# Performance work log

Hardware: AMD Instinct MI355X
Metric: run time of the kernel (lower is better)

## Reference

```python
import jax, jax.numpy as jnp
import numpy as np


def setup_inputs() -> dict:
    key = jax.random.key(0)
    k1, k2, k3 = jax.random.split(key, 3)
    batch, d_in, d_out, b = 8192, 4096, 4096, 128
    k_in, k_out = d_in // b, d_out // b  # 32, 32
    x = jax.random.normal(k1, (batch, d_in), dtype=jnp.float32)
    W = jax.random.normal(k2, (k_out, k_in, b), dtype=jnp.float32) * 0.1
    d_bernoulli = jnp.ones((d_in,), dtype=jnp.float32)
    bias = jax.random.normal(k3, (d_out,), dtype=jnp.float32) * 0.1
    return {"x": x, "W": W, "d_bernoulli": d_bernoulli, "bias": bias}


def reference(x, W, d_bernoulli, bias):
    # Block-circulant matmul via FFT convolution theorem, fully batched.
    # W: (k_out, k_in, b); each W[i, j] is the first row of a circulant block.
    batch, d_in = x.shape
    k_out, k_in, b = W.shape
    xd = x * d_bernoulli[None, :]
    # d_in == k_in * b here (divisible), so no padding needed.
    x_blocks = xd.reshape(batch, k_in, b)
    Xf = jnp.fft.fft(x_blocks, axis=-1)               # (batch, k_in, b) complex
    Wf = jnp.conjugate(jnp.fft.fft(W, axis=-1))       # (k_out, k_in, b) complex
    # sum over input blocks j in frequency domain, then one IFFT per output block
    Yf = jnp.einsum("bjn,ijn->bin", Xf, Wf)           # (batch, k_out, b)
    y = jnp.fft.ifft(Yf, axis=-1).real.reshape(batch, k_out * b)
    return y + bias[None, :]
```

## Files before the change

### kernel.cpp

```cpp
#include <hip/hip_runtime.h>
#include <hip/hip_bf16.h>
#include <stdint.h>

typedef __bf16 bf16x8 __attribute__((ext_vector_type(8)));
typedef float  f32x4  __attribute__((ext_vector_type(4)));

#define MDIM 8192
#define NDIM 4096
#define KDIM 4096
#define BM   256
#define BN   256
#define BK   64
#define NT   (KDIM / BK)

__device__ __forceinline__ void lds_load16(const void* gsrc, void* ldst) {
    __builtin_amdgcn_global_load_lds(
        (const __attribute__((address_space(1))) unsigned int*)gsrc,
        (__attribute__((address_space(3)))       unsigned int*)ldst,
        16, 0, 0);
}

__global__ __launch_bounds__(256) void cvt_x(const float* __restrict__ X,
                                             __bf16* __restrict__ Xb) {
    size_t t  = (size_t)blockIdx.x * blockDim.x + threadIdx.x;
    size_t i0 = t * 8;
    float4 a = *(const float4*)(X + i0);
    float4 b = *(const float4*)(X + i0 + 4);
    bf16x8 o;
    o[0] = (__bf16)a.x; o[1] = (__bf16)a.y; o[2] = (__bf16)a.z; o[3] = (__bf16)a.w;
    o[4] = (__bf16)b.x; o[5] = (__bf16)b.y; o[6] = (__bf16)b.z; o[7] = (__bf16)b.w;
    *(bf16x8*)(Xb + i0) = o;
}

__global__ __launch_bounds__(256) void build_bt(const float* __restrict__ W,
                                                const float* __restrict__ d,
                                                __bf16* __restrict__ Bt) {
    int t  = blockIdx.x * blockDim.x + threadIdx.x;
    int c  = t >> 9;
    int k0 = (t & 511) * 8;
    int i  = c  >> 7;
    int j  = k0 >> 7;
    const float* wp = W + ((size_t)i * 32 + j) * 128;
    bf16x8 o;
#pragma unroll
    for (int e = 0; e < 8; ++e) {
        int k = k0 + e;
        float v = wp[(k - c) & 127] * d[k];
        o[e] = (__bf16)v;
    }
    *(bf16x8*)(Bt + (size_t)c * KDIM + k0) = o;
}

__global__ __launch_bounds__(512, 2) void gemm_bc(const __bf16* __restrict__ A,
                                                  const __bf16* __restrict__ Bt,
                                                  const float* __restrict__ bias,
                                                  float* __restrict__ C) {
    __shared__ __align__(16) char lds[2 * 65536];

    const int bid = blockIdx.x;
    const int cpx = gridDim.x >> 3;
    const int swz = (bid & 7) * cpx + (bid >> 3);
    const int ntn = NDIM / BN;
    const int brow = (swz / ntn) * BM;
    const int bcol = (swz % ntn) * BN;

    const int tid  = threadIdx.x;
    const int wid  = tid >> 6;
    const int lane = tid & 63;
    const int wr   = wid >> 2;
    const int wc   = wid & 3;
    const int rlo  = lane & 15;
    const int kg   = lane >> 4;

    const int xorK = (rlo & 7) << 4;
    const int kb0  = ((kg * 16)      ^ xorK);
    const int kb1  = ((64 + kg * 16) ^ xorK);
    const char* bufA0 = lds + wr * 16384 + rlo * 128;
    const char* bufB0 = lds + 32768 + (wc >> 1) * 16384 + ((wc & 1) * 64 + rlo) * 128;

    const int sRow = wid * 8 + (lane >> 3);
    const int sCol = 8 * ((lane & 7) ^ ((lane >> 3) & 7));

    const __bf16* Abase = A  + (size_t)brow * KDIM;
    const __bf16* Bbase = Bt + (size_t)bcol * KDIM;

    auto stageA = [&](int t_, int half, int par_) {
#pragma unroll
        for (int l = 0; l < 2; ++l) {
            const __bf16* gp = Abase + (size_t)(half * 128 + l * 64 + sRow) * KDIM
                               + t_ * 64 + sCol;
            lds_load16(gp, lds + par_ * 65536 + half * 16384 + l * 8192 + wid * 1024);
        }
    };
    auto stageB = [&](int t_, int half, int par_) {
#pragma unroll
        for (int l = 0; l < 2; ++l) {
            const __bf16* gp = Bbase + (size_t)(half * 128 + l * 64 + sRow) * KDIM
                               + t_ * 64 + sCol;
            lds_load16(gp, lds + par_ * 65536 + 32768 + half * 16384 + l * 8192 + wid * 1024);
        }
    };

    f32x4 acc[8][4];
#pragma unroll
    for (int i = 0; i < 8; ++i)
#pragma unroll
        for (int j = 0; j < 4; ++j) acc[i][j] = (f32x4)0.0f;

    stageA(0, 0, 0); stageA(0, 1, 0);
    stageB(0, 0, 0); stageB(0, 1, 0);
    stageB(1, 0, 1); stageB(1, 1, 1);

    bf16x8 bf[4][2];

#define PHASE(q, STAGE_STMT)                                                        \
    {                                                                               \
        bf16x8 a00 = *(const bf16x8*)(bufA + (q) * 4096 +    0 + kb0);              \
        bf16x8 a01 = *(const bf16x8*)(bufA + (q) * 4096 +    0 + kb1);              \
        bf16x8 a10 = *(const bf16x8*)(bufA + (q) * 4096 + 2048 + kb0);              \
        bf16x8 a11 = *(const bf16x8*)(bufA + (q) * 4096 + 2048 + kb1);              \
        STAGE_STMT;                                                                 \
        __builtin_amdgcn_s_barrier();                                               \
        asm volatile("s_waitcnt lgkmcnt(0)" ::: "memory");                          \
        __builtin_amdgcn_s_setprio(1);                                              \
        _Pragma("unroll")                                                           \
        for (int j = 0; j < 4; ++j) {                                               \
            acc[(q)*2+0][j] = __builtin_amdgcn_mfma_f32_16x16x32_bf16(a00, bf[j][0], acc[(q)*2+0][j], 0, 0, 0); \
            acc[(q)*2+0][j] = __builtin_amdgcn_mfma_f32_16x16x32_bf16(a01, bf[j][1], acc[(q)*2+0][j], 0, 0, 0); \
            acc[(q)*2+1][j] = __builtin_amdgcn_mfma_f32_16x16x32_bf16(a10, bf[j][0], acc[(q)*2+1][j], 0, 0, 0); \
            acc[(q)*2+1][j] = __builtin_amdgcn_mfma_f32_16x16x32_bf16(a11, bf[j][1], acc[(q)*2+1][j], 0, 0, 0); \
        }                                                                           \
        __builtin_amdgcn_s_setprio(0);                                              \
    }

    for (int t = 0; t < NT; ++t) {
        const int par = t & 1;
        const char* bufA = bufA0 + par * 65536;
        const char* bufB = bufB0 + par * 65536;

        if (t < NT - 1) {
            asm volatile("s_waitcnt vmcnt(4)" ::: "memory");
        } else {
            asm volatile("s_waitcnt vmcnt(0)" ::: "memory");
        }
        __builtin_amdgcn_s_barrier();

#pragma unroll
        for (int j = 0; j < 4; ++j) {
            bf[j][0] = *(const bf16x8*)(bufB + j * 2048 + kb0);
            bf[j][1] = *(const bf16x8*)(bufB + j * 2048 + kb1);
        }
        PHASE(0, { if (t + 1 < NT) stageA(t + 1, 0, 1 - par); });
        PHASE(1, { if (t + 1 < NT) stageA(t + 1, 1, 1 - par); });
        PHASE(2, { if (t + 2 < NT) stageB(t + 2, 0, par); });
        PHASE(3, { if (t + 2 < NT) stageB(t + 2, 1, par); });
    }
#undef PHASE

#pragma unroll
    for (int j = 0; j < 4; ++j) {
        const int col = bcol + wc * 64 + j * 16 + rlo;
        const float bs = bias[col];
#pragma unroll
        for (int i = 0; i < 8; ++i) {
            const int row = brow + wr * 128 + i * 16 + kg * 4;
#pragma unroll
            for (int r = 0; r < 4; ++r)
                C[(size_t)(row + r) * NDIM + col] = acc[i][j][r] + bs;
        }
    }
}

extern "C" void kernel_launch(void* const* d_in, const int* in_sizes, int n_in,
                              void* d_out, int out_size, void* d_ws, size_t ws_size,
                              hipStream_t stream) {
    const float* x    = (const float*)d_in[0];
    const float* W    = (const float*)d_in[1];
    const float* d    = (const float*)d_in[2];
    const float* bias = (const float*)d_in[3];
    float* y = (float*)d_out;

    __bf16* Xb = (__bf16*)d_ws;
    __bf16* Bt = (__bf16*)((char*)d_ws + (size_t)MDIM * KDIM * 2);

    cvt_x<<<(MDIM * (size_t)KDIM) / 8 / 256, 256, 0, stream>>>(x, Xb);
    build_bt<<<(NDIM * KDIM) / 8 / 256, 256, 0, stream>>>(W, d, Bt);
    gemm_bc<<<(MDIM / BM) * (NDIM / BN), 512, 0, stream>>>(Xb, Bt, bias, y);
}
```

Before: 283.7 us.

## Switch GEMM inner loop to 32x32x16 bf16 MFMA with two-phase schedule

Replaces the 16x16x32 MFMA tiling with 32x32x16 MFMA instructions. Each wave now holds 4x2 accumulators of 16 floats, and the LDS fragment addressing and the epilogue row mapping are reworked to match. The four-phase per-K-step schedule is collapsed into two phases, each with its own barrier and prefetch stage, which cuts barriers and LDS reads per MFMA flop. The larger MFMA shape improves operand reuse from LDS, at the cost of different register pressure and a coarser overlap between LDS loads and compute.

```diff
diff --git a/kernel.cpp b/kernel.cpp
--- a/kernel.cpp
+++ b/kernel.cpp
@@ -2,8 +2,8 @@
 #include <hip/hip_bf16.h>
 #include <stdint.h>
 
-typedef __bf16 bf16x8 __attribute__((ext_vector_type(8)));
-typedef float  f32x4  __attribute__((ext_vector_type(4)));
+typedef __bf16 bf16x8  __attribute__((ext_vector_type(8)));
+typedef float  f32x16  __attribute__((ext_vector_type(16)));
 
 #define MDIM 8192
 #define NDIM 4096
@@ -69,14 +69,13 @@
     const int lane = tid & 63;
     const int wr   = wid >> 2;
     const int wc   = wid & 3;
-    const int rlo  = lane & 15;
-    const int kg   = lane >> 4;
+    const int l31  = lane & 31;
+    const int kh   = lane >> 5;
 
-    const int xorK = (rlo & 7) << 4;
-    const int kb0  = ((kg * 16)      ^ xorK);
-    const int kb1  = ((64 + kg * 16) ^ xorK);
-    const char* bufA0 = lds + wr * 16384 + rlo * 128;
-    const char* bufB0 = lds + 32768 + (wc >> 1) * 16384 + ((wc & 1) * 64 + rlo) * 128;
+    const int kbase = (((l31 & 7) ^ kh) << 4);
+
+    const int aOffBase = (wr * 128 + l31) * 128;
+    const int bOffBase = 32768 + (wc * 64 + l31) * 128;
 
     const int sRow = wid * 8 + (lane >> 3);
     const int sCol = 8 * ((lane & 7) ^ ((lane >> 3) & 7));
@@ -101,72 +100,77 @@
         }
     };
 
-    f32x4 acc[8][4];
+    f32x16 acc[4][2];
 #pragma unroll
-    for (int i = 0; i < 8; ++i)
+    for (int i = 0; i < 4; ++i)
 #pragma unroll
-        for (int j = 0; j < 4; ++j) acc[i][j] = (f32x4)0.0f;
+        for (int j = 0; j < 2; ++j) acc[i][j] = (f32x16)0.0f;
 
     stageA(0, 0, 0); stageA(0, 1, 0);
     stageB(0, 0, 0); stageB(0, 1, 0);
     stageB(1, 0, 1); stageB(1, 1, 1);
 
-    bf16x8 bf[4][2];
+    for (int t = 0; t < NT; ++t) {
+        const int par  = t & 1;
+        const char* buf = lds + par * 65536;
 
-#define PHASE(q, STAGE_STMT)                                                        \
-    {                                                                               \
-        bf16x8 a00 = *(const bf16x8*)(bufA + (q) * 4096 +    0 + kb0);              \
-        bf16x8 a01 = *(const bf16x8*)(bufA + (q) * 4096 +    0 + kb1);              \
-        bf16x8 a10 = *(const bf16x8*)(bufA + (q) * 4096 + 2048 + kb0);              \
-        bf16x8 a11 = *(const bf16x8*)(bufA + (q) * 4096 + 2048 + kb1);              \
-        STAGE_STMT;                                                                 \
-        __builtin_amdgcn_s_barrier();                                               \
-        asm volatile("s_waitcnt lgkmcnt(0)" ::: "memory");                          \
-        __builtin_amdgcn_s_setprio(1);                                              \
-        _Pragma("unroll")                                                           \
-        for (int j = 0; j < 4; ++j) {                                               \
-            acc[(q)*2+0][j] = __builtin_amdgcn_mfma_f32_16x16x32_bf16(a00, bf[j][0], acc[(q)*2+0][j], 0, 0, 0); \
-            acc[(q)*2+0][j] = __builtin_amdgcn_mfma_f32_16x16x32_bf16(a01, bf[j][1], acc[(q)*2+0][j], 0, 0, 0); \
-            acc[(q)*2+1][j] = __builtin_amdgcn_mfma_f32_16x16x32_bf16(a10, bf[j][0], acc[(q)*2+1][j], 0, 0, 0); \
-            acc[(q)*2+1][j] = __builtin_amdgcn_mfma_f32_16x16x32_bf16(a11, bf[j][1], acc[(q)*2+1][j], 0, 0, 0); \
-        }                                                                           \
-        __builtin_amdgcn_s_setprio(0);                                              \
+        if (t < NT - 1) { asm volatile("s_waitcnt vmcnt(4)" ::: "memory"); }
+        else            { asm volatile("s_waitcnt vmcnt(0)" ::: "memory"); }
+        __builtin_amdgcn_s_barrier();
+
+        bf16x8 bfr[2][4], a0[4], a1[4];
+#pragma unroll
+        for (int s = 0; s < 4; ++s) {
+            bfr[0][s] = *(const bf16x8*)(buf + bOffBase +    0 + ((s << 5) ^ kbase));
+            bfr[1][s] = *(const bf16x8*)(buf + bOffBase + 4096 + ((s << 5) ^ kbase));
+            a0[s]     = *(const bf16x8*)(buf + aOffBase +    0 + ((s << 5) ^ kbase));
+            a1[s]     = *(const bf16x8*)(buf + aOffBase + 4096 + ((s << 5) ^ kbase));
+        }
+        if (t + 1 < NT) { stageA(t + 1, 0, 1 - par); stageA(t + 1, 1, 1 - par); }
+        __builtin_amdgcn_s_barrier();
+        asm volatile("s_waitcnt lgkmcnt(0)" ::: "memory");
+        __builtin_amdgcn_s_setprio(1);
+#pragma unroll
+        for (int s = 0; s < 4; ++s) {
+            acc[0][0] = __builtin_amdgcn_mfma_f32_32x32x16_bf16(a0[s], bfr[0][s], acc[0][0], 0, 0, 0);
+            acc[0][1] = __builtin_amdgcn_mfma_f32_32x32x16_bf16(a0[s], bfr[1][s], acc[0][1], 0, 0, 0);
+            acc[1][0] = __builtin_amdgcn_mfma_f32_32x32x16_bf16(a1[s], bfr[0][s], acc[1][0], 0, 0, 0);
+            acc[1][1] = __builtin_amdgcn_mfma_f32_32x32x16_bf16(a1[s], bfr[1][s], acc[1][1], 0, 0, 0);
+        }
+        __builtin_amdgcn_s_setprio(0);
+
+        bf16x8 a2[4], a3[4];
+#pragma unroll
+        for (int s = 0; s < 4; ++s) {
+            a2[s] = *(const bf16x8*)(buf + aOffBase +  8192 + ((s << 5) ^ kbase));
+            a3[s] = *(const bf16x8*)(buf + aOffBase + 12288 + ((s << 5) ^ kbase));
+        }
+        __builtin_amdgcn_s_barrier();
+        if (t + 2 < NT) { stageB(t + 2, 0, par); stageB(t + 2, 1, par); }
+        asm volatile("s_waitcnt lgkmcnt(0)" ::: "memory");
+        __builtin_amdgcn_s_setprio(1);
+#pragma unroll
+        for (int s = 0; s < 4; ++s) {
+            acc[2][0] = __builtin_amdgcn_mfma_f32_32x32x16_bf16(a2[s], bfr[0][s], acc[2][0], 0, 0, 0);
+            acc[2][1] = __builtin_amdgcn_mfma_f32_32x32x16_bf16(a2[s], bfr[1][s], acc[2][1], 0, 0, 0);
+            acc[3][0] = __builtin_amdgcn_mfma_f32_32x32x16_bf16(a3[s], bfr[0][s], acc[3][0], 0, 0, 0);
+            acc[3][1] = __builtin_amdgcn_mfma_f32_32x32x16_bf16(a3[s], bfr[1][s], acc[3][1], 0, 0, 0);
+        }
+        __builtin_amdgcn_s_setprio(0);
     }
 
-    for (int t = 0; t < NT; ++t) {
-        const int par = t & 1;
-        const char* bufA = bufA0 + par * 65536;
-        const char* bufB = bufB0 + par * 65536;
-
-        if (t < NT - 1) {
-            asm volatile("s_waitcnt vmcnt(4)" ::: "memory");
-        } else {
-            asm volatile("s_waitcnt vmcnt(0)" ::: "memory");
-        }
-        __builtin_amdgcn_s_barrier();
-
 #pragma unroll
-        for (int j = 0; j < 4; ++j) {
-            bf[j][0] = *(const bf16x8*)(bufB + j * 2048 + kb0);
-            bf[j][1] = *(const bf16x8*)(bufB + j * 2048 + kb1);
-        }
-        PHASE(0, { if (t + 1 < NT) stageA(t + 1, 0, 1 - par); });
-        PHASE(1, { if (t + 1 < NT) stageA(t + 1, 1, 1 - par); });
-        PHASE(2, { if (t + 2 < NT) stageB(t + 2, 0, par); });
-        PHASE(3, { if (t + 2 < NT) stageB(t + 2, 1, par); });
-    }
-#undef PHASE
-
-#pragma unroll
-    for (int j = 0; j < 4; ++j) {
-        const int col = bcol + wc * 64 + j * 16 + rlo;
+    for (int j = 0; j < 2; ++j) {
+        const int col = bcol + wc * 64 + j * 32 + l31;
         const float bs = bias[col];
 #pragma unroll
-        for (int i = 0; i < 8; ++i) {
-            const int row = brow + wr * 128 + i * 16 + kg * 4;
+        for (int i = 0; i < 4; ++i) {
+            const int rb = brow + wr * 128 + i * 32 + 4 * kh;
 #pragma unroll
-            for (int r = 0; r < 4; ++r)
-                C[(size_t)(row + r) * NDIM + col] = acc[i][j][r] + bs;
+            for (int r = 0; r < 16; ++r) {
+                const int row = rb + (r & 3) + 8 * (r >> 2);
+                C[(size_t)row * NDIM + col] = acc[i][j][r] + bs;
+            }
         }
     }
 }
```

New measurement: 324.1 us. 1.14x slower.

## Restructure GEMM main loop with per-phase double barriers and end-of-iteration vmcnt wait

Applied to the files above, without the earlier changes.

Reorganizes the GEMM k-loop into four explicit phases, each bracketed by barriers before and after its MFMA block. The global-load wait moves from the top of the iteration to the end of the last phase, with a prologue wait added, and the loop is unrolled by 2. The goal is to keep waves in lockstep, ping-pong style, so that LDS reads, global-to-LDS staging and MFMA bursts overlap better across the waves. In exchange it adds extra barriers per iteration, which could introduce stalls.

```diff
diff --git a/kernel.cpp b/kernel.cpp
--- a/kernel.cpp
+++ b/kernel.cpp
@@ -110,52 +110,83 @@
     stageA(0, 0, 0); stageA(0, 1, 0);
     stageB(0, 0, 0); stageB(0, 1, 0);
     stageB(1, 0, 1); stageB(1, 1, 1);
+    asm volatile("s_waitcnt vmcnt(4)" ::: "memory");
+    __builtin_amdgcn_s_barrier();
 
     bf16x8 bf[4][2];
 
-#define PHASE(q, STAGE_STMT)                                                        \
-    {                                                                               \
-        bf16x8 a00 = *(const bf16x8*)(bufA + (q) * 4096 +    0 + kb0);              \
-        bf16x8 a01 = *(const bf16x8*)(bufA + (q) * 4096 +    0 + kb1);              \
-        bf16x8 a10 = *(const bf16x8*)(bufA + (q) * 4096 + 2048 + kb0);              \
-        bf16x8 a11 = *(const bf16x8*)(bufA + (q) * 4096 + 2048 + kb1);              \
-        STAGE_STMT;                                                                 \
-        __builtin_amdgcn_s_barrier();                                               \
-        asm volatile("s_waitcnt lgkmcnt(0)" ::: "memory");                          \
-        __builtin_amdgcn_s_setprio(1);                                              \
-        _Pragma("unroll")                                                           \
-        for (int j = 0; j < 4; ++j) {                                               \
-            acc[(q)*2+0][j] = __builtin_amdgcn_mfma_f32_16x16x32_bf16(a00, bf[j][0], acc[(q)*2+0][j], 0, 0, 0); \
-            acc[(q)*2+0][j] = __builtin_amdgcn_mfma_f32_16x16x32_bf16(a01, bf[j][1], acc[(q)*2+0][j], 0, 0, 0); \
-            acc[(q)*2+1][j] = __builtin_amdgcn_mfma_f32_16x16x32_bf16(a10, bf[j][0], acc[(q)*2+1][j], 0, 0, 0); \
-            acc[(q)*2+1][j] = __builtin_amdgcn_mfma_f32_16x16x32_bf16(a11, bf[j][1], acc[(q)*2+1][j], 0, 0, 0); \
-        }                                                                           \
-        __builtin_amdgcn_s_setprio(0);                                              \
-    }
-
+#define MFMA16(q)                                                                   \
+    _Pragma("unroll")                                                               \
+    for (int j = 0; j < 4; ++j) {                                                   \
+        acc[(q)*2+0][j] = __builtin_amdgcn_mfma_f32_16x16x32_bf16(a00, bf[j][0], acc[(q)*2+0][j], 0, 0, 0); \
+        acc[(q)*2+0][j] = __builtin_amdgcn_mfma_f32_16x16x32_bf16(a01, bf[j][1], acc[(q)*2+0][j], 0, 0, 0); \
+        acc[(q)*2+1][j] = __builtin_amdgcn_mfma_f32_16x16x32_bf16(a10, bf[j][0], acc[(q)*2+1][j], 0, 0, 0); \
+        acc[(q)*2+1][j] = __builtin_amdgcn_mfma_f32_16x16x32_bf16(a11, bf[j][1], acc[(q)*2+1][j], 0, 0, 0); \
+    }
+
+#define READ_A(q)                                                                   \
+    bf16x8 a00 = *(const bf16x8*)(bufA + (q) * 4096 +    0 + kb0);                  \
+    bf16x8 a01 = *(const bf16x8*)(bufA + (q) * 4096 +    0 + kb1);                  \
+    bf16x8 a10 = *(const bf16x8*)(bufA + (q) * 4096 + 2048 + kb0);                  \
+    bf16x8 a11 = *(const bf16x8*)(bufA + (q) * 4096 + 2048 + kb1);
+
+#pragma unroll 2
     for (int t = 0; t < NT; ++t) {
         const int par = t & 1;
         const char* bufA = bufA0 + par * 65536;
         const char* bufB = bufB0 + par * 65536;
 
-        if (t < NT - 1) {
-            asm volatile("s_waitcnt vmcnt(4)" ::: "memory");
-        } else {
-            asm volatile("s_waitcnt vmcnt(0)" ::: "memory");
-        }
-        __builtin_amdgcn_s_barrier();
-
-#pragma unroll
-        for (int j = 0; j < 4; ++j) {
-            bf[j][0] = *(const bf16x8*)(bufB + j * 2048 + kb0);
-            bf[j][1] = *(const bf16x8*)(bufB + j * 2048 + kb1);
-        }
-        PHASE(0, { if (t + 1 < NT) stageA(t + 1, 0, 1 - par); });
-        PHASE(1, { if (t + 1 < NT) stageA(t + 1, 1, 1 - par); });
-        PHASE(2, { if (t + 2 < NT) stageB(t + 2, 0, par); });
-        PHASE(3, { if (t + 2 < NT) stageB(t + 2, 1, par); });
-    }
-#undef PHASE
+        {
+#pragma unroll
+            for (int j = 0; j < 4; ++j) {
+                bf[j][0] = *(const bf16x8*)(bufB + j * 2048 + kb0);
+                bf[j][1] = *(const bf16x8*)(bufB + j * 2048 + kb1);
+            }
+            READ_A(0)
+            if (t + 1 < NT) stageA(t + 1, 0, 1 - par);
+            asm volatile("s_waitcnt lgkmcnt(8)" ::: "memory");
+            __builtin_amdgcn_s_barrier();
+            asm volatile("s_waitcnt lgkmcnt(0)" ::: "memory");
+            __builtin_amdgcn_s_setprio(1);
+            MFMA16(0)
+            __builtin_amdgcn_s_setprio(0);
+            __builtin_amdgcn_s_barrier();
+        }
+        {
+            READ_A(1)
+            if (t + 1 < NT) stageA(t + 1, 1, 1 - par);
+            __builtin_amdgcn_s_barrier();
+            asm volatile("s_waitcnt lgkmcnt(0)" ::: "memory");
+            __builtin_amdgcn_s_setprio(1);
+            MFMA16(1)
+            __builtin_amdgcn_s_setprio(0);
+            __builtin_amdgcn_s_barrier();
+        }
+        {
+            READ_A(2)
+            if (t + 2 < NT) stageB(t + 2, 0, par);
+            __builtin_amdgcn_s_barrier();
+            asm volatile("s_waitcnt lgkmcnt(0)" ::: "memory");
+            __builtin_amdgcn_s_setprio(1);
+            MFMA16(2)
+            __builtin_amdgcn_s_setprio(0);
+            __builtin_amdgcn_s_barrier();
+        }
+        {
+            READ_A(3)
+            if (t + 2 < NT) stageB(t + 2, 1, par);
+            __builtin_amdgcn_s_barrier();
+            asm volatile("s_waitcnt lgkmcnt(0)" ::: "memory");
+            __builtin_amdgcn_s_setprio(1);
+            MFMA16(3)
+            __builtin_amdgcn_s_setprio(0);
+            if (t < NT - 2)       { asm volatile("s_waitcnt vmcnt(4)" ::: "memory"); }
+            else if (t == NT - 2) { asm volatile("s_waitcnt vmcnt(0)" ::: "memory"); }
+            __builtin_amdgcn_s_barrier();
+        }
+    }
+#undef MFMA16
+#undef READ_A
 
 #pragma unroll
     for (int j = 0; j < 4; ++j) {
```

Result: slower. 296.4 us (+4.5%).
